# Kernel optimization log

Hardware: AMD Instinct MI355X
Metric: run time of the kernel (lower is better)

Reference implementation:

```python
import jax, jax.numpy as jnp
import numpy as np
import math

B, S, HID = 2, 2048, 1024
NH = 16
HD = HID // NH          # 64
VD = HD // 2            # 32 value dim
TD = HD - VD            # 32 type dim
EPS = 1e-6


def setup_inputs() -> dict:
    key = jax.random.key(0)
    ks = jax.random.split(key, 12)
    std = 1.0 / math.sqrt(HID)
    xav = math.sqrt(6.0 / (TD + TD))
    return {
        "x": jax.random.normal(ks[0], (B, S, HID), dtype=jnp.float32),
        "q_w": jax.random.uniform(ks[1], (HID, HID), jnp.float32, -std, std),
        "q_b": jax.random.uniform(ks[2], (HID,), jnp.float32, -std, std),
        "k_w": jax.random.uniform(ks[3], (HID, HID), jnp.float32, -std, std),
        "k_b": jax.random.uniform(ks[4], (HID,), jnp.float32, -std, std),
        "v_w": jax.random.uniform(ks[5], (HID, HID), jnp.float32, -std, std),
        "v_b": jax.random.uniform(ks[6], (HID,), jnp.float32, -std, std),
        "out_w": jax.random.uniform(ks[7], (HID, HID), jnp.float32, -std, std),
        "out_b": jax.random.uniform(ks[8], (HID,), jnp.float32, -std, std),
        "type_bilinear": jax.random.uniform(ks[9], (NH, TD, TD), jnp.float32, -xav, xav),
        "type_bias": jnp.full((NH,), 2.0, dtype=jnp.float32),
        "mask": jnp.ones((B, S), dtype=jnp.int32),
    }


def reference(x, q_w, q_b, k_w, k_b, v_w, v_b, out_w, out_b, type_bilinear, type_bias, mask):
    # projections: [B,S,HID] -> [B,NH,S,HD]
    def proj(w, b):
        y = jnp.einsum("bsi,io->bso", x, w) + b
        return y.reshape(B, S, NH, HD).transpose(0, 2, 1, 3)

    q = proj(q_w, q_b)
    k = proj(k_w, k_b)
    v = proj(v_w, v_b)

    q_val, q_type = q[..., :VD], q[..., VD:]
    k_val, k_type = k[..., :VD], k[..., VD:]

    # standard value score: [B,NH,S,S]
    val_scores = jnp.einsum("bhqd,bhkd->bhqk", q_val, k_val) / math.sqrt(VD)

    # per-head bilinear type score: q_type @ W_h @ k_type^T + bias_h
    qt = jnp.einsum("bhqd,hde->bhqe", q_type, type_bilinear)
    type_scores = jnp.einsum("bhqe,bhke->bhqk", qt, k_type) + type_bias[None, :, None, None]
    type_unif = jax.nn.sigmoid(type_scores)

    scores = val_scores + jnp.log(type_unif + EPS)

    # mask: [B,S] -> broadcast over heads and query dim (keys masked)
    m = (mask[:, None, None, :] != 0)
    scores = jnp.where(m, scores, -jnp.inf)

    attn = jax.nn.softmax(scores, axis=-1)
    out = jnp.einsum("bhqk,bhkd->bhqd", attn, v)          # [B,NH,S,HD]
    out = out.transpose(0, 2, 1, 3).reshape(B, S, HID)
    return jnp.einsum("bsi,io->bso", out, out_w) + out_b
```

## Files before the change

### kernel.cpp

```cpp
#include <hip/hip_runtime.h>
#include <hip/hip_bf16.h>
#include <math.h>

typedef __attribute__((ext_vector_type(8))) short bf16x8;
typedef __attribute__((ext_vector_type(4))) float f32x4;
typedef __attribute__((ext_vector_type(4))) int   i32x4;

#define NHh 16
#define Sq  2048
#define HIDq 1024
#define HDq 64
#define LOG2E 1.4426950408889634f

#if __has_builtin(__builtin_amdgcn_exp2f)
#define EXP2F(x) __builtin_amdgcn_exp2f(x)
#else
#define EXP2F(x) exp2f(x)
#endif
#if __has_builtin(__builtin_amdgcn_rcpf)
#define RCPF(x) __builtin_amdgcn_rcpf(x)
#else
#define RCPF(x) (1.0f/(x))
#endif

__device__ __forceinline__ unsigned short f2bf(float f){
  union { float f; unsigned u; } v; v.f = f;
  unsigned r = v.u + 0x7fffu + ((v.u >> 16) & 1u);
  return (unsigned short)(r >> 16);
}
__device__ __forceinline__ float bf2f(unsigned short s){
  union { unsigned u; float f; } v; v.u = ((unsigned)s) << 16;
  return v.f;
}
__device__ __forceinline__ unsigned pk2bf(float lo, float hi){
  union { __hip_bfloat162 h; unsigned u; } w;
  w.h = __float22bfloat162_rn(make_float2(lo, hi));
  return w.u;
}

__device__ __forceinline__ void gload_lds16(const unsigned short* g, unsigned short* l){
  __builtin_amdgcn_global_load_lds(
      (const __attribute__((address_space(1))) unsigned int*)g,
      (__attribute__((address_space(3))) unsigned int*)l, 16, 0, 0);
}

__global__ __launch_bounds__(256) void convert_x(const float* __restrict__ in,
                                                 unsigned short* __restrict__ out, int n8,
                                                 const int* __restrict__ mask,
                                                 float* __restrict__ Mf){
  int bid = blockIdx.x;
  int nmain = gridDim.x - 2;
  if (bid >= nmain){
    int base = (bid - nmain)*2048 + threadIdx.x*8;
    #pragma unroll
    for (int j=0;j<8;j++) Mf[base+j] = mask[base+j] ? 0.f : -1e30f;
    return;
  }
  int i = bid*256 + threadIdx.x;
  if (i >= n8) return;
  const f32x4* p = (const f32x4*)(in + (size_t)i*8);
  f32x4 a = p[0], b = p[1];
  union { unsigned short us[8]; i32x4 v; } o;
  #pragma unroll
  for (int j=0;j<4;j++){ o.us[j] = f2bf(a[j]); o.us[4+j] = f2bf(b[j]); }
  *(i32x4*)(out + (size_t)i*8) = o.v;
}

__global__ __launch_bounds__(256) void transpose_w(const float* __restrict__ w0, const float* __restrict__ w1,
                                                   const float* __restrict__ w2, const float* __restrict__ w3,
                                                   unsigned short* __restrict__ wT){
  __shared__ float tile[32][33];
  int z = blockIdx.z;
  const float* w = (z==0)?w0:(z==1)?w1:(z==2)?w2:w3;
  unsigned short* dst = wT + (size_t)z*HIDq*HIDq;
  int tx = threadIdx.x, ty = threadIdx.y;
  int n0 = blockIdx.x*32, k0 = blockIdx.y*32;
  #pragma unroll
  for (int i=ty;i<32;i+=8) tile[i][tx] = w[(size_t)(k0+i)*HIDq + n0+tx];
  __syncthreads();
  #pragma unroll
  for (int i=ty;i<32;i+=8) dst[(size_t)(n0+i)*HIDq + k0+tx] = f2bf(tile[tx][i]);
}

__device__ __forceinline__ void gemm_core_gl(const unsigned short* __restrict__ Ag,
                                             const unsigned short* __restrict__ Bg,
                                             unsigned short* As, unsigned short* Bs,
                                             int t, int wv, int lane, int wr, int wc, int lr, int g,
                                             f32x4 acc[4][4]){
  for (int k0=0; k0<HIDq; k0+=64){
    __syncthreads();
    #pragma unroll
    for (int j=0;j<4;j++){
      int flat = (j*4+wv)*64 + lane;
      int row = flat>>3, c = flat&7;
      int srcc = (c ^ (row&7))*8;
      gload_lds16(Ag + (size_t)row*HIDq + k0 + srcc, &As[flat*8]);
      gload_lds16(Bg + (size_t)row*HIDq + k0 + srcc, &Bs[flat*8]);
    }
    __syncthreads();
    #pragma unroll
    for (int ks=0; ks<2; ks++){
      bf16x8 af[4], bfv[4];
      #pragma unroll
      for (int m=0;m<4;m++){
        int rr = wr + m*16 + lr;
        af[m]  = *(bf16x8*)&As[rr*64 + (((ks*4+g) ^ (rr&7))*8)];
      }
      #pragma unroll
      for (int n=0;n<4;n++){
        int rr = wc + n*16 + lr;
        bfv[n] = *(bf16x8*)&Bs[rr*64 + (((ks*4+g) ^ (rr&7))*8)];
      }
      #pragma unroll
      for (int n=0;n<4;n++)
        #pragma unroll
        for (int m=0;m<4;m++)
          acc[n][m] = __builtin_amdgcn_mfma_f32_16x16x32_bf16(bfv[n], af[m], acc[n][m], 0,0,0);
    }
  }
}

__global__ __launch_bounds__(256) void gemm_qkv(const unsigned short* __restrict__ xbf,
    const unsigned short* __restrict__ wT,
    const float* __restrict__ q_b, const float* __restrict__ k_b, const float* __restrict__ v_b,
    unsigned short* __restrict__ Qeff, unsigned short* __restrict__ Keff,
    unsigned short* __restrict__ Vt){
  __shared__ unsigned short As[128*64];
  __shared__ unsigned short Bs[128*64];
  const int t = threadIdx.x;
  const int wv = t>>6, lane = t&63, g = lane>>4, lr = lane&15;
  const int wr = (wv>>1)*64, wc = (wv&1)*64;
  f32x4 acc[4][4] = {};
  const int xb = blockIdx.x, yb = blockIdx.y;
  const float VS = 0.25501335f;

  if (xb < 16){
    const int row0 = yb*128, col0 = xb*128;
    gemm_core_gl(xbf + (size_t)row0*HIDq, wT + (size_t)col0*HIDq, As, Bs, t, wv, lane, wr, wc, lr, g, acc);
    #pragma unroll
    for (int n=0;n<4;n++){
      #pragma unroll
      for (int m=0;m<4;m++){
        int row = row0 + wr + m*16 + lr;
        int b_ = row>>11, ss = row&2047;
        int colb = col0 + wc + n*16 + g*4;
        int seg = colb>>10, cw = colb&1023;
        int hh = cw>>6, d = cw&63;
        const float* bp = seg ? k_b : q_b;
        f32x4 bb = *(const f32x4*)&bp[cw];
        float sc = seg ? 1.0f : (d < 32 ? VS : -LOG2E);
        unsigned short* E = seg ? Keff : Qeff;
        float v0 = (acc[n][m][0]+bb[0])*sc, v1 = (acc[n][m][1]+bb[1])*sc;
        float v2 = (acc[n][m][2]+bb[2])*sc, v3 = (acc[n][m][3]+bb[3])*sc;
        union { unsigned u[2]; unsigned long long ll; } W;
        W.u[0] = pk2bf(v0,v1); W.u[1] = pk2bf(v2,v3);
        *(unsigned long long*)&E[(((size_t)b_*NHh+hh)*Sq+ss)*HDq + d] = W.ll;
      }
    }
  } else {
    const int row0 = (xb-16)*128, col0 = yb*128;
    gemm_core_gl(wT + (size_t)2*HIDq*HIDq + (size_t)row0*HIDq, xbf + (size_t)col0*HIDq,
                 As, Bs, t, wv, lane, wr, wc, lr, g, acc);
    #pragma unroll
    for (int n=0;n<4;n++){
      #pragma unroll
      for (int m=0;m<4;m++){
        int chan = row0 + wr + m*16 + lr;
        int hh = chan>>6, d = chan&63;
        float bv = v_b[chan];
        int colb = col0 + wc + n*16 + g*4;
        int b_ = colb>>11, ss = colb&2047;
        union { unsigned u[2]; unsigned long long ll; } W;
        W.u[0] = pk2bf(acc[n][m][0]+bv, acc[n][m][1]+bv);
        W.u[1] = pk2bf(acc[n][m][2]+bv, acc[n][m][3]+bv);
        *(unsigned long long*)&Vt[(((size_t)b_*NHh+hh)*HDq + d)*Sq + ss] = W.ll;
      }
    }
  }
}

__global__ __launch_bounds__(256) void gemm_out(const unsigned short* __restrict__ A,
                                                const unsigned short* __restrict__ Bt,
                                                const float* __restrict__ bias,
                                                float* __restrict__ C){
  __shared__ unsigned short As[128*64];
  __shared__ unsigned short Bs[128*64];
  const int t = threadIdx.x;
  const int wv = t>>6, lane = t&63, g = lane>>4, lr = lane&15;
  const int wr = (wv>>1)*64, wc = (wv&1)*64;
  const int row0 = blockIdx.y*128, col0 = blockIdx.x*128;
  f32x4 acc[4][4] = {};
  gemm_core_gl(A + (size_t)row0*HIDq, Bt + (size_t)col0*HIDq, As, Bs, t, wv, lane, wr, wc, lr, g, acc);
  #pragma unroll
  for (int n=0;n<4;n++){
    #pragma unroll
    for (int m=0;m<4;m++){
      int row = row0 + wr + m*16 + lr;
      int colb = col0 + wc + n*16 + g*4;
      f32x4 bb = *(const f32x4*)&bias[colb];
      f32x4 o = acc[n][m] + bb;
      *(f32x4*)&C[(size_t)row*HIDq + colb] = o;
    }
  }
}

__global__ __launch_bounds__(512,2) void attn_kernel(
    const unsigned short* __restrict__ Qe, const unsigned short* __restrict__ Ke,
    const unsigned short* __restrict__ Vt, const float* __restrict__ Tb,
    const float* __restrict__ tbias, const float* __restrict__ Mf,
    unsigned short* __restrict__ Obuf)
{
  __shared__ __align__(16) unsigned char smem[81920];
  unsigned short* Ks0 = (unsigned short*)smem;
  unsigned short* Vs0 = (unsigned short*)(smem + 16384);
  unsigned short* Ks1 = (unsigned short*)(smem + 32768);
  unsigned short* Vs1 = (unsigned short*)(smem + 49152);
  unsigned short* Pl  = (unsigned short*)(smem + 65536);
  float* qls = (float*)(smem + 32768);
  unsigned short* qtls = Pl;

  const int t = threadIdx.x;
  const int dd = blockIdx.x;
  const int slot = dd>>3, xcd = dd&7;
  const int x = slot & 15;
  const int bh = ((slot>>4)<<3) | xcd;
  const int h = bh & 15, b = bh >> 4;
  const int q0 = x*128;
  const int wv = t>>6, lane = t&63, g = lane>>4, lr = lane&15;

  const unsigned short* Qb  = Qe + (((size_t)b*NHh+h)*Sq + q0)*HDq;
  const unsigned short* Kb  = Ke + ((size_t)b*NHh+h)*(size_t)Sq*HDq;
  const unsigned short* Vtb = Vt + ((size_t)b*NHh+h)*(size_t)HDq*Sq;
  const float* Mfb = Mf + (size_t)b*Sq;

  const int ch0 = (wv*2+0)*64 + lane, ch1 = (wv*2+1)*64 + lane;

  {
    int kr0 = ch0>>3, kc0 = ch0&7, kr1 = ch1>>3, kc1 = ch1&7;
    gload_lds16(Kb + (size_t)kr0*HDq + (kc0 ^ (kr0&7))*8, Ks0 + ch0*8);
    gload_lds16(Kb + (size_t)kr1*HDq + (kc1 ^ (kr1&7))*8, Ks0 + ch1*8);
    int vd0 = ch0>>4, vc0 = ch0&15, vd1 = ch1>>4, vc1 = ch1&15;
    gload_lds16(Vtb + (size_t)vd0*Sq + (vc0 ^ (vd0&15))*8, Vs0 + ch0*8);
    gload_lds16(Vtb + (size_t)vd1*Sq + (vc1 ^ (vd1&15))*8, Vs0 + ch1*8);
  }

  {
    int row = t>>2, c8 = (t&3)*8;
    bf16x8 v = *(const bf16x8*)(Qb + (size_t)row*HDq + 32 + c8);
    #pragma unroll
    for (int j=0;j<8;j++) qls[row*33 + c8 + j] = bf2f((unsigned short)v[j]);
  }
  __syncthreads();
  {
    int row = t&127, e0 = (t>>7)*8;
    const float* Th = Tb + (size_t)h*1024;
    float a[8] = {};
    #pragma unroll 4
    for (int d=0; d<32; d++){
      float qd = qls[row*33 + d];
      const f32x4* tp = (const f32x4*)(Th + d*32 + e0);
      f32x4 t0 = tp[0], t1 = tp[1];
      a[0]+=qd*t0[0]; a[1]+=qd*t0[1]; a[2]+=qd*t0[2]; a[3]+=qd*t0[3];
      a[4]+=qd*t1[0]; a[5]+=qd*t1[1]; a[6]+=qd*t1[2]; a[7]+=qd*t1[3];
    }
    __syncthreads();
    union { unsigned u[2]; unsigned long long ll; } W0, W1;
    W0.u[0]=pk2bf(a[0],a[1]); W0.u[1]=pk2bf(a[2],a[3]);
    W1.u[0]=pk2bf(a[4],a[5]); W1.u[1]=pk2bf(a[6],a[7]);
    *(unsigned long long*)&qtls[row*40 + e0]     = W0.ll;
    *(unsigned long long*)&qtls[row*40 + e0 + 4] = W1.ll;
  }
  bf16x8 qvf = *(const bf16x8*)(Qb + (size_t)(wv*16+lr)*HDq + g*8);
  __syncthreads();
  bf16x8 qtn = *(const bf16x8*)&qtls[(wv*16+lr)*40 + g*8];
  __syncthreads();

  const float tbn = -tbias[h]*LOG2E;
  const f32x4 tbc = {tbn,tbn,tbn,tbn};
  f32x4 oT[4] = {};
  f32x4 lsum = {0.f,0.f,0.f,0.f};
  unsigned short* Pw = &Pl[wv*1024 + lr*64];
  const int swp = (lr&7)*8;
  bf16x8 onesf;
  #pragma unroll
  for (int j=0;j<8;j++) onesf[j] = (short)0x3F80;

  unsigned short *Kc = Ks0, *Vc = Vs0, *Kn = Ks1, *Vn = Vs1;

  for (int kt=0; kt<Sq; kt+=128){
    f32x4 madd[2][4];
    #pragma unroll
    for (int kh2=0; kh2<2; kh2++)
      #pragma unroll
      for (int ks=0; ks<4; ks++)
        madd[kh2][ks] = *(const f32x4*)(Mfb + kt + kh2*64 + ks*16 + g*4);
    if (kt + 128 < Sq){
      int kt2 = kt + 128;
      int kr0 = ch0>>3, kc0 = ch0&7, kr1 = ch1>>3, kc1 = ch1&7;
      gload_lds16(Kb + (size_t)(kt2+kr0)*HDq + (kc0 ^ (kr0&7))*8, Kn + ch0*8);
      gload_lds16(Kb + (size_t)(kt2+kr1)*HDq + (kc1 ^ (kr1&7))*8, Kn + ch1*8);
      int vd0 = ch0>>4, vc0 = ch0&15, vd1 = ch1>>4, vc1 = ch1&15;
      gload_lds16(Vtb + (size_t)vd0*Sq + kt2 + (vc0 ^ (vd0&15))*8, Vn + ch0*8);
      gload_lds16(Vtb + (size_t)vd1*Sq + kt2 + (vc1 ^ (vd1&15))*8, Vn + ch1*8);
    }

    #pragma unroll
    for (int kh=0; kh<2; kh++){
      f32x4 sv[4], st[4];
      __builtin_amdgcn_s_setprio(1);
      #pragma unroll
      for (int ks=0; ks<4; ks++){
        int krow = kh*64 + ks*16 + lr;
        const unsigned short* kb = &Kc[krow*64];
        int sw = (krow&7)*8;
        bf16x8 kf0 = *(const bf16x8*)(kb + ((g*8) ^ sw));
        bf16x8 kf1 = *(const bf16x8*)(kb + ((32 + g*8) ^ sw));
        sv[ks] = __builtin_amdgcn_mfma_f32_16x16x32_bf16(kf0, qvf, madd[kh][ks], 0,0,0);
        st[ks] = __builtin_amdgcn_mfma_f32_16x16x32_bf16(kf1, qtn, tbc, 0,0,0);
      }
      __builtin_amdgcn_s_setprio(0);
      #pragma unroll
      for (int ks=0; ks<4; ks++){
        float p0 = EXP2F(sv[ks][0]) * RCPF(1.f + EXP2F(st[ks][0]));
        float p1 = EXP2F(sv[ks][1]) * RCPF(1.f + EXP2F(st[ks][1]));
        float p2 = EXP2F(sv[ks][2]) * RCPF(1.f + EXP2F(st[ks][2]));
        float p3 = EXP2F(sv[ks][3]) * RCPF(1.f + EXP2F(st[ks][3]));
        union { unsigned u[2]; unsigned long long ll; } W;
        W.u[0] = pk2bf(p0,p1); W.u[1] = pk2bf(p2,p3);
        *(unsigned long long*)(Pw + ((ks*16 + g*4) ^ swp)) = W.ll;
      }
      #pragma unroll
      for (int ks2=0; ks2<2; ks2++){
        bf16x8 pf = *(const bf16x8*)(Pw + ((ks2*32 + g*8) ^ swp));
        __builtin_amdgcn_s_setprio(1);
        lsum = __builtin_amdgcn_mfma_f32_16x16x32_bf16(onesf, pf, lsum, 0,0,0);
        #pragma unroll
        for (int db=0; db<4; db++){
          int vrow = db*16 + lr;
          bf16x8 vf = *(const bf16x8*)(&Vc[vrow*128] + ((kh*64 + ks2*32 + g*8) ^ ((vrow&15)*8)));
          oT[db] = __builtin_amdgcn_mfma_f32_16x16x32_bf16(vf, pf, oT[db], 0,0,0);
        }
        __builtin_amdgcn_s_setprio(0);
      }
    }
    __syncthreads();
    unsigned short* tp;
    tp = Kc; Kc = Kn; Kn = tp;
    tp = Vc; Vc = Vn; Vn = tp;
  }

  float linv = (lsum[0] > 0.f) ? RCPF(lsum[0]) : 0.f;
  int srow = q0 + wv*16 + lr;
  unsigned short* Ob = Obuf + ((size_t)b*Sq + srow)*HIDq + h*HDq;
  #pragma unroll
  for (int db=0; db<4; db++){
    union { unsigned u[2]; unsigned long long ll; } W;
    W.u[0] = pk2bf(oT[db][0]*linv, oT[db][1]*linv);
    W.u[1] = pk2bf(oT[db][2]*linv, oT[db][3]*linv);
    *(unsigned long long*)(Ob + db*16 + g*4) = W.ll;
  }
}

extern "C" void kernel_launch(void* const* d_in, const int* in_sizes, int n_in,
                              void* d_out, int out_size, void* d_ws, size_t ws_size,
                              hipStream_t stream) {
  const float* x     = (const float*)d_in[0];
  const float* q_w   = (const float*)d_in[1];
  const float* q_b   = (const float*)d_in[2];
  const float* k_w   = (const float*)d_in[3];
  const float* k_b   = (const float*)d_in[4];
  const float* v_w   = (const float*)d_in[5];
  const float* v_b   = (const float*)d_in[6];
  const float* out_w = (const float*)d_in[7];
  const float* out_b = (const float*)d_in[8];
  const float* Tb    = (const float*)d_in[9];
  const float* tbias = (const float*)d_in[10];
  const int*   mask  = (const int*)d_in[11];

  const size_t MROWS = 4096;
  unsigned short* xbf  = (unsigned short*)d_ws;
  unsigned short* wT   = xbf  + MROWS*HIDq;
  unsigned short* Qeff = wT   + (size_t)4*HIDq*HIDq;
  unsigned short* Keff = Qeff + MROWS*HIDq;
  unsigned short* Vt   = Keff + MROWS*HIDq;
  unsigned short* Obuf = Vt   + MROWS*HIDq;
  float*          Mf   = (float*)(Obuf + MROWS*HIDq);

  int n8 = (int)(MROWS*HIDq/8);
  convert_x<<<dim3(n8/256 + 2), dim3(256), 0, stream>>>(x, xbf, n8, mask, Mf);
  transpose_w<<<dim3(32,32,4), dim3(32,8), 0, stream>>>(q_w, k_w, v_w, out_w, wT);

  gemm_qkv<<<dim3(24,32), dim3(256), 0, stream>>>(xbf, wT, q_b, k_b, v_b, Qeff, Keff, Vt);

  attn_kernel<<<dim3(512), dim3(512), 0, stream>>>(Qeff, Keff, Vt, Tb, tbias, Mf, Obuf);

  gemm_out<<<dim3(8,32), dim3(256), 0, stream>>>(Obuf, wT + (size_t)3*HIDq*HIDq, out_b, (float*)d_out);
}
```

Before: 159.6 us.

## Shrink attention blocks to 64 queries and stage 64-key K/V tiles

The attention kernel now runs 1024 blocks of 256 threads, each covering 64 query rows instead of 128, and stages K/V in 64-key tiles with a two-phase double buffer inside each 128-key iteration. LDS use drops from 80KB to 40KB, so more blocks can be resident per CU, giving more latency hiding and finer scheduling granularity. In exchange each K/V tile is loaded by twice as many blocks, doubling global/L2 traffic for K and V, and there are twice as many barriers per key range. The initial K/V prefetch is also moved after the Q-type projection so the overlapped qls buffer is not overwritten.

Result: no change. 160.3 us (+0.4%).

```diff
diff --git a/kernel.cpp b/kernel.cpp
--- a/kernel.cpp
+++ b/kernel.cpp
@@ -204,28 +204,28 @@
   }
 }
 
-__global__ __launch_bounds__(512,2) void attn_kernel(
+__global__ __launch_bounds__(256,4) void attn_kernel(
     const unsigned short* __restrict__ Qe, const unsigned short* __restrict__ Ke,
     const unsigned short* __restrict__ Vt, const float* __restrict__ Tb,
     const float* __restrict__ tbias, const float* __restrict__ Mf,
     unsigned short* __restrict__ Obuf)
 {
-  __shared__ __align__(16) unsigned char smem[81920];
+  __shared__ __align__(16) unsigned char smem[40960];
   unsigned short* Ks0 = (unsigned short*)smem;
+  unsigned short* Ks1 = (unsigned short*)(smem + 8192);
   unsigned short* Vs0 = (unsigned short*)(smem + 16384);
-  unsigned short* Ks1 = (unsigned short*)(smem + 32768);
-  unsigned short* Vs1 = (unsigned short*)(smem + 49152);
-  unsigned short* Pl  = (unsigned short*)(smem + 65536);
-  float* qls = (float*)(smem + 32768);
+  unsigned short* Vs1 = (unsigned short*)(smem + 24576);
+  unsigned short* Pl  = (unsigned short*)(smem + 32768);
+  float* qls = (float*)smem;
   unsigned short* qtls = Pl;
 
   const int t = threadIdx.x;
   const int dd = blockIdx.x;
   const int slot = dd>>3, xcd = dd&7;
-  const int x = slot & 15;
-  const int bh = ((slot>>4)<<3) | xcd;
+  const int x = slot & 31;
+  const int bh = ((slot>>5)<<3) | xcd;
   const int h = bh & 15, b = bh >> 4;
-  const int q0 = x*128;
+  const int q0 = x*64;
   const int wv = t>>6, lane = t&63, g = lane>>4, lr = lane&15;
 
   const unsigned short* Qb  = Qe + (((size_t)b*NHh+h)*Sq + q0)*HDq;
@@ -233,17 +233,6 @@
   const unsigned short* Vtb = Vt + ((size_t)b*NHh+h)*(size_t)HDq*Sq;
   const float* Mfb = Mf + (size_t)b*Sq;
 
-  const int ch0 = (wv*2+0)*64 + lane, ch1 = (wv*2+1)*64 + lane;
-
-  {
-    int kr0 = ch0>>3, kc0 = ch0&7, kr1 = ch1>>3, kc1 = ch1&7;
-    gload_lds16(Kb + (size_t)kr0*HDq + (kc0 ^ (kr0&7))*8, Ks0 + ch0*8);
-    gload_lds16(Kb + (size_t)kr1*HDq + (kc1 ^ (kr1&7))*8, Ks0 + ch1*8);
-    int vd0 = ch0>>4, vc0 = ch0&15, vd1 = ch1>>4, vc1 = ch1&15;
-    gload_lds16(Vtb + (size_t)vd0*Sq + (vc0 ^ (vd0&15))*8, Vs0 + ch0*8);
-    gload_lds16(Vtb + (size_t)vd1*Sq + (vc1 ^ (vd1&15))*8, Vs0 + ch1*8);
-  }
-
   {
     int row = t>>2, c8 = (t&3)*8;
     bf16x8 v = *(const bf16x8*)(Qb + (size_t)row*HDq + 32 + c8);
@@ -252,7 +241,7 @@
   }
   __syncthreads();
   {
-    int row = t&127, e0 = (t>>7)*8;
+    int row = t&63, e0 = (t>>6)*8;
     const float* Th = Tb + (size_t)h*1024;
     float a[8] = {};
     #pragma unroll 4
@@ -263,7 +252,6 @@
       a[0]+=qd*t0[0]; a[1]+=qd*t0[1]; a[2]+=qd*t0[2]; a[3]+=qd*t0[3];
       a[4]+=qd*t1[0]; a[5]+=qd*t1[1]; a[6]+=qd*t1[2]; a[7]+=qd*t1[3];
     }
-    __syncthreads();
     union { unsigned u[2]; unsigned long long ll; } W0, W1;
     W0.u[0]=pk2bf(a[0],a[1]); W0.u[1]=pk2bf(a[2],a[3]);
     W1.u[0]=pk2bf(a[4],a[5]); W1.u[1]=pk2bf(a[6],a[7]);
@@ -273,6 +261,15 @@
   bf16x8 qvf = *(const bf16x8*)(Qb + (size_t)(wv*16+lr)*HDq + g*8);
   __syncthreads();
   bf16x8 qtn = *(const bf16x8*)&qtls[(wv*16+lr)*40 + g*8];
+
+  #pragma unroll
+  for (int i=0;i<2;i++){
+    int c = t + i*256;
+    int kr = c>>3, kc = c&7;
+    gload_lds16(Kb + (size_t)kr*HDq + ((kc ^ (kr&7))*8), Ks0 + c*8);
+    int vd = c>>3, vc = c&7;
+    gload_lds16(Vtb + (size_t)vd*Sq + ((vc ^ (vd&7))*8), Vs0 + c*8);
+  }
   __syncthreads();
 
   const float tbn = -tbias[h]*LOG2E;
@@ -285,68 +282,62 @@
   #pragma unroll
   for (int j=0;j<8;j++) onesf[j] = (short)0x3F80;
 
-  unsigned short *Kc = Ks0, *Vc = Vs0, *Kn = Ks1, *Vn = Vs1;
+  auto phase = [&](const unsigned short* Kc, const unsigned short* Vc, int key0,
+                   bool doStage, int key0n, unsigned short* Kn, unsigned short* Vn){
+    f32x4 madd[4];
+    #pragma unroll
+    for (int ks=0; ks<4; ks++)
+      madd[ks] = *(const f32x4*)(Mfb + key0 + ks*16 + g*4);
+    if (doStage){
+      #pragma unroll
+      for (int i=0;i<2;i++){
+        int c = t + i*256;
+        int kr = c>>3, kc = c&7;
+        gload_lds16(Kb + (size_t)(key0n+kr)*HDq + ((kc ^ (kr&7))*8), Kn + c*8);
+        int vd = c>>3, vc = c&7;
+        gload_lds16(Vtb + (size_t)vd*Sq + key0n + ((vc ^ (vd&7))*8), Vn + c*8);
+      }
+    }
+    f32x4 sv[4], st[4];
+    __builtin_amdgcn_s_setprio(1);
+    #pragma unroll
+    for (int ks=0; ks<4; ks++){
+      const unsigned short* kb = Kc + (ks*16+lr)*64;
+      bf16x8 kf0 = *(const bf16x8*)(kb + (((g  ) ^ (lr&7))*8));
+      bf16x8 kf1 = *(const bf16x8*)(kb + (((4+g) ^ (lr&7))*8));
+      sv[ks] = __builtin_amdgcn_mfma_f32_16x16x32_bf16(kf0, qvf, madd[ks], 0,0,0);
+      st[ks] = __builtin_amdgcn_mfma_f32_16x16x32_bf16(kf1, qtn, tbc, 0,0,0);
+    }
+    __builtin_amdgcn_s_setprio(0);
+    #pragma unroll
+    for (int ks=0; ks<4; ks++){
+      float p0 = EXP2F(sv[ks][0]) * RCPF(1.f + EXP2F(st[ks][0]));
+      float p1 = EXP2F(sv[ks][1]) * RCPF(1.f + EXP2F(st[ks][1]));
+      float p2 = EXP2F(sv[ks][2]) * RCPF(1.f + EXP2F(st[ks][2]));
+      float p3 = EXP2F(sv[ks][3]) * RCPF(1.f + EXP2F(st[ks][3]));
+      union { unsigned u[2]; unsigned long long ll; } W;
+      W.u[0] = pk2bf(p0,p1); W.u[1] = pk2bf(p2,p3);
+      *(unsigned long long*)(Pw + ((ks*16 + g*4) ^ swp)) = W.ll;
+    }
+    #pragma unroll
+    for (int ks2=0; ks2<2; ks2++){
+      bf16x8 pf = *(const bf16x8*)(Pw + ((ks2*32 + g*8) ^ swp));
+      __builtin_amdgcn_s_setprio(1);
+      lsum = __builtin_amdgcn_mfma_f32_16x16x32_bf16(onesf, pf, lsum, 0,0,0);
+      #pragma unroll
+      for (int db=0; db<4; db++){
+        bf16x8 vf = *(const bf16x8*)(Vc + (db*16+lr)*64 + (((ks2*4+g) ^ (lr&7))*8));
+        oT[db] = __builtin_amdgcn_mfma_f32_16x16x32_bf16(vf, pf, oT[db], 0,0,0);
+      }
+      __builtin_amdgcn_s_setprio(0);
+    }
+  };
 
   for (int kt=0; kt<Sq; kt+=128){
-    f32x4 madd[2][4];
-    #pragma unroll
-    for (int kh2=0; kh2<2; kh2++)
-      #pragma unroll
-      for (int ks=0; ks<4; ks++)
-        madd[kh2][ks] = *(const f32x4*)(Mfb + kt + kh2*64 + ks*16 + g*4);
-    if (kt + 128 < Sq){
-      int kt2 = kt + 128;
-      int kr0 = ch0>>3, kc0 = ch0&7, kr1 = ch1>>3, kc1 = ch1&7;
-      gload_lds16(Kb + (size_t)(kt2+kr0)*HDq + (kc0 ^ (kr0&7))*8, Kn + ch0*8);
-      gload_lds16(Kb + (size_t)(kt2+kr1)*HDq + (kc1 ^ (kr1&7))*8, Kn + ch1*8);
-      int vd0 = ch0>>4, vc0 = ch0&15, vd1 = ch1>>4, vc1 = ch1&15;
-      gload_lds16(Vtb + (size_t)vd0*Sq + kt2 + (vc0 ^ (vd0&15))*8, Vn + ch0*8);
-      gload_lds16(Vtb + (size_t)vd1*Sq + kt2 + (vc1 ^ (vd1&15))*8, Vn + ch1*8);
-    }
-
-    #pragma unroll
-    for (int kh=0; kh<2; kh++){
-      f32x4 sv[4], st[4];
-      __builtin_amdgcn_s_setprio(1);
-      #pragma unroll
-      for (int ks=0; ks<4; ks++){
-        int krow = kh*64 + ks*16 + lr;
-        const unsigned short* kb = &Kc[krow*64];
-        int sw = (krow&7)*8;
-        bf16x8 kf0 = *(const bf16x8*)(kb + ((g*8) ^ sw));
-        bf16x8 kf1 = *(const bf16x8*)(kb + ((32 + g*8) ^ sw));
-        sv[ks] = __builtin_amdgcn_mfma_f32_16x16x32_bf16(kf0, qvf, madd[kh][ks], 0,0,0);
-        st[ks] = __builtin_amdgcn_mfma_f32_16x16x32_bf16(kf1, qtn, tbc, 0,0,0);
-      }
-      __builtin_amdgcn_s_setprio(0);
-      #pragma unroll
-      for (int ks=0; ks<4; ks++){
-        float p0 = EXP2F(sv[ks][0]) * RCPF(1.f + EXP2F(st[ks][0]));
-        float p1 = EXP2F(sv[ks][1]) * RCPF(1.f + EXP2F(st[ks][1]));
-        float p2 = EXP2F(sv[ks][2]) * RCPF(1.f + EXP2F(st[ks][2]));
-        float p3 = EXP2F(sv[ks][3]) * RCPF(1.f + EXP2F(st[ks][3]));
-        union { unsigned u[2]; unsigned long long ll; } W;
-        W.u[0] = pk2bf(p0,p1); W.u[1] = pk2bf(p2,p3);
-        *(unsigned long long*)(Pw + ((ks*16 + g*4) ^ swp)) = W.ll;
-      }
-      #pragma unroll
-      for (int ks2=0; ks2<2; ks2++){
-        bf16x8 pf = *(const bf16x8*)(Pw + ((ks2*32 + g*8) ^ swp));
-        __builtin_amdgcn_s_setprio(1);
-        lsum = __builtin_amdgcn_mfma_f32_16x16x32_bf16(onesf, pf, lsum, 0,0,0);
-        #pragma unroll
-        for (int db=0; db<4; db++){
-          int vrow = db*16 + lr;
-          bf16x8 vf = *(const bf16x8*)(&Vc[vrow*128] + ((kh*64 + ks2*32 + g*8) ^ ((vrow&15)*8)));
-          oT[db] = __builtin_amdgcn_mfma_f32_16x16x32_bf16(vf, pf, oT[db], 0,0,0);
-        }
-        __builtin_amdgcn_s_setprio(0);
-      }
-    }
+    phase(Ks0, Vs0, kt,      true,           kt+64,  Ks1, Vs1);
     __syncthreads();
-    unsigned short* tp;
-    tp = Kc; Kc = Kn; Kn = tp;
-    tp = Vc; Vc = Vn; Vn = tp;
+    phase(Ks1, Vs1, kt+64,   kt+128 < Sq,    kt+128, Ks0, Vs0);
+    __syncthreads();
   }
 
   float linv = (lsum[0] > 0.f) ? RCPF(lsum[0]) : 0.f;
@@ -392,7 +383,7 @@
 
   gemm_qkv<<<dim3(24,32), dim3(256), 0, stream>>>(xbf, wT, q_b, k_b, v_b, Qeff, Keff, Vt);
 
-  attn_kernel<<<dim3(512), dim3(512), 0, stream>>>(Qeff, Keff, Vt, Tb, tbias, Mf, Obuf);
+  attn_kernel<<<dim3(1024), dim3(256), 0, stream>>>(Qeff, Keff, Vt, Tb, tbias, Mf, Obuf);
 
   gemm_out<<<dim3(8,32), dim3(256), 0, stream>>>(Obuf, wT + (size_t)3*HIDq*HIDq, out_b, (float*)d_out);
 }
```
